# Kernel tuning notes

Hardware: AMD Instinct MI355X
Metric: run time of the kernel (lower is better)

The kernel has to match this reference:

```python
import jax, jax.numpy as jnp
import numpy as np

# ---- static config (matches init_kwargs) ----
OC, IC, K, S, PAD = 128, 64, 3, 1, 1
M, T, R = 5, 8, 2.5            # ALSH m, table_size, LSH bucket width r
SPAN = K * K * IC              # kernel_span = 576


def setup_inputs() -> dict:
    key = jax.random.key(0)
    k1, k2, k3, k4 = jax.random.split(key, 4)
    # xavier_uniform on the (OC, SPAN) kernel matrix
    bound = float(np.sqrt(6.0 / (OC + SPAN)))
    kernels = jax.random.uniform(k1, (OC, SPAN), minval=-bound, maxval=bound, dtype=jnp.float32)
    a = jax.random.normal(k2, (SPAN + M,), dtype=jnp.float32)          # LSH projection
    b = jax.random.uniform(k3, (), minval=0.0, maxval=R, dtype=jnp.float32)  # LSH offset
    x = jax.random.normal(k4, (16, IC, 56, 56), dtype=jnp.float32)
    return {"x": x, "kernels": kernels, "a": a, "b": b, "mode": 0}


def _im2col(x):
    # [B, SPAN, H2, W2] with feature order (C, kh, kw)
    p = jax.lax.conv_general_dilated_patches(x, (K, K), (S, S), [(PAD, PAD), (PAD, PAD)])
    B, _, H2, W2 = p.shape
    # patch matrix [SPAN, B*H2*W2]
    return p.transpose(1, 0, 2, 3).reshape(SPAN, -1), B, H2, W2


def _bucket(h):
    # floor((h+b)/r); fmod table_size; abs  (matches torch .fmod_ then .abs_)
    return jnp.abs(jnp.fmod(h.astype(jnp.int32), T))


def reference(x, kernels, a, b, mode):
    patch_matr, B, H2, W2 = _im2col(x)            # [SPAN, N], N = B*H2*W2

    # ---- vote: hash every patch column with Q-augmentation (append m halves) ----
    v = a[:SPAN] @ patch_matr + 0.5 * jnp.sum(a[SPAN:])      # [N]
    votes = _bucket(jnp.floor((v + b) / R))
    counts = jnp.zeros((T,), jnp.int32).at[votes].add(1)
    bucket = jnp.argmax(counts)                               # most common bucket

    # ---- hash table: hash each kernel row with P-augmentation (norm powers) ----
    norms2 = jnp.sum(kernels * kernels, axis=1)               # ||k||^2, [OC]
    powers = jnp.stack([norms2 ** (2 ** i) for i in range(M)], axis=1)  # ||k||^{2,4,...,2^M}
    hk = kernels @ a[:SPAN] + powers @ a[SPAN:]               # [OC]
    kidx = _bucket(jnp.floor((hk + b) / R))                   # bucket of each kernel

    # ---- select kernels in the winning bucket; scale by |rows|/OC ----
    mask = (kidx == bucket).astype(x.dtype)                   # [OC]
    cnt = jnp.sum(mask)
    # original gathers the selected rows (variable oc); we scatter back to the
    # full OC channels (zeros for inactive kernels) for static shapes.
    # empty bucket -> dense conv with all kernels, no rescale.
    factor = jnp.where(cnt > 0, mask * (OC / jnp.maximum(cnt, 1.0)), jnp.ones_like(mask))

    out = (kernels * factor[:, None]) @ patch_matr            # [OC, N]
    out = out.reshape(OC, B, H2 * W2).transpose(1, 0, 2)
    return out.reshape(B, OC, H2, W2)
```

## Files before the change

### kernel.cpp

```cpp
#include <hip/hip_runtime.h>
#include <math.h>

#define IC 64
#define OC 128
#define HH 56
#define WW 56
#define BATCH 16
#define HP 58
#define HW (HH*WW)
#define NPIX (BATCH*HW)
#define SPAN 576
#define TSIZE 8
#define VBANDS 28
#define VBLOCKS (BATCH*VBANDS)
#define W2BASE  VBLOCKS
#define BORDBASE (VBLOCKS + OC)
#define NBLK1 (BORDBASE + BATCH)

typedef unsigned short ushort_t;
typedef unsigned int uint_t;
typedef __attribute__((ext_vector_type(8))) __bf16 bf16x8;
typedef __attribute__((ext_vector_type(4))) float f32x4;

__device__ __forceinline__ ushort_t bf16_rne(float f) {
  uint_t u = __builtin_bit_cast(uint_t, f);
  u += 0x7FFFu + ((u >> 16) & 1u);
  return (ushort_t)(u >> 16);
}

__global__ __launch_bounds__(256)
void prep_kernel(const float* __restrict__ x, const float* __restrict__ kernels,
                 const float* __restrict__ a, const float* __restrict__ bptr,
                 ushort_t* __restrict__ xpad, ushort_t* __restrict__ w2m,
                 int* __restrict__ rbucket, int* __restrict__ hist_partial) {
  __shared__ float tl[224 * 9];
  __shared__ ushort_t lx[112 * 66];
  __shared__ int hist[TSIZE];
  __shared__ float red0[256], red1[256];
  const int bx = blockIdx.x, t = threadIdx.x;

  if (bx < VBLOCKS) {
    const int b = bx / VBANDS, band = bx % VBANDS;
    const int r0 = band * 2;
    if (t < TSIZE) hist[t] = 0;
    if (t < 224) {
      const int prow = r0 - 1 + t / 56;
      const int col = t % 56;
      const bool inr = ((unsigned)prow < (unsigned)HH);
      const bool mid = (t >= 56 && t < 168);
      const float* xb = x + (size_t)b * IC * HW + (inr ? prow * WW + col : 0);
      ushort_t* lxp = lx + (mid ? (t - 56) : 0) * 66;
      float t9[9] = {0, 0, 0, 0, 0, 0, 0, 0, 0};
      #pragma unroll 8
      for (int c = 0; c < IC; ++c) {
        float xv = inr ? xb[(size_t)c * HW] : 0.0f;
        #pragma unroll
        for (int tap = 0; tap < 9; ++tap) t9[tap] += a[c * 9 + tap] * xv;
        if (mid) lxp[c] = bf16_rne(xv);
      }
      #pragma unroll
      for (int tap = 0; tap < 9; ++tap) tl[t * 9 + tap] = t9[tap];
    }
    __syncthreads();
    if (t < 112) {
      int lr = t / 56, col = t % 56;
      float v = 0.0f;
      #pragma unroll
      for (int kh = 0; kh < 3; ++kh) {
        int gr = r0 + lr - 1 + kh;
        #pragma unroll
        for (int kw = 0; kw < 3; ++kw) {
          int cc = col - 1 + kw;
          if ((unsigned)gr < (unsigned)HH && (unsigned)cc < (unsigned)WW)
            v += tl[((lr + kh) * 56 + cc) * 9 + (kh * 3 + kw)];
        }
      }
      float tail = 0.5f * (a[576] + a[577] + a[578] + a[579] + a[580]);
      int hi = (int)floorf((v + tail + bptr[0]) / 2.5f);
      int r = hi % TSIZE;
      if (r < 0) r = -r;
      atomicAdd(&hist[r], 1);
    }
    {
      const uint_t* lxu = (const uint_t*)lx;
      uint_t* xp = (uint_t*)xpad;
      #pragma unroll
      for (int j = 0; j < 14; ++j) {
        int idx = j * 256 + t;
        int px = idx >> 5, cp = idx & 31;
        int lr = px / 56, c0 = px % 56;
        int y = r0 + 1 + lr, xw = c0 + 1;
        xp[(((size_t)(b * HP + y)) * HP + xw) * 32 + cp] = lxu[px * 33 + cp];
      }
    }
    __syncthreads();
    if (t < TSIZE) hist_partial[bx * TSIZE + t] = hist[t];
  } else if (bx < BORDBASE) {
    const int r = bx - W2BASE;
    const float* row = kernels + (size_t)r * SPAN;
    float d = 0.0f, n2 = 0.0f;
    #pragma unroll
    for (int k0 = 0; k0 < 3; ++k0) {
      int k = k0 * 256 + t;
      if (k < SPAN) { float kv = row[k]; d += kv * a[k]; n2 += kv * kv; }
    }
    red0[t] = d; red1[t] = n2;
    __syncthreads();
    for (int s = 128; s > 0; s >>= 1) {
      if (t < s) { red0[t] += red0[t + s]; red1[t] += red1[t + s]; }
      __syncthreads();
    }
    if (t == 0) {
      float hk = red0[0], p = red1[0];
      #pragma unroll
      for (int i = 0; i < 5; ++i) { hk += p * a[SPAN + i]; p = p * p; }
      int hi = (int)floorf((hk + bptr[0]) / 2.5f);
      int rr = hi % TSIZE;
      if (rr < 0) rr = -rr;
      rbucket[r] = rr;
    }
    #pragma unroll
    for (int j0 = 0; j0 < 3; ++j0) {
      int j = j0 * 256 + t;
      if (j < SPAN) {
        int tap = j / 64, rem = j % 64;
        int chunk = rem >> 3, c = rem & 7;
        w2m[(size_t)tap * 8192 + (r >> 4) * 1024 + chunk * 128 + (r & 15) * 8 + c] =
            bf16_rne(row[rem * 9 + tap]);
      }
    }
  } else {
    const int ib = bx - BORDBASE;
    uint_t* xp = (uint_t*)xpad + (size_t)ib * HP * HP * 32;
    for (int j = t; j < 7296; j += 256) {
      int px = j >> 5, cp = j & 31;
      int y, xw;
      if (px < 58) { y = 0; xw = px; }
      else if (px < 116) { y = 57; xw = px - 58; }
      else { int k = px - 116; y = 1 + (k >> 1); xw = (k & 1) * 57; }
      xp[((size_t)y * HP + xw) * 32 + cp] = 0;
    }
  }
}

__global__ __launch_bounds__(256, 4)
void gemm_kernel(const ushort_t* __restrict__ w2m, const ushort_t* __restrict__ xpad,
                 const int* __restrict__ hist_partial, const int* __restrict__ rbucket,
                 float* __restrict__ out) {
  __shared__ ushort_t As[8192];
  __shared__ ushort_t Bs[4096];
  __shared__ float factor_s[OC];
  __shared__ int counts_s[TSIZE];
  __shared__ int cnt_w[4];
  const int tid = threadIdx.x;
  const int wave = tid >> 6, lane = tid & 63;
  const int n0 = blockIdx.x * 64;

  int aseg[4];
  #pragma unroll
  for (int i = 0; i < 4; ++i) aseg[i] = (wave * 4 + i) * 512 + lane * 8;

  int bg;
  {
    int p = n0 + wave * 16 + (lane & 15);
    int b = p / HW, rem = p % HW;
    int h = rem / WW, w = rem % WW;
    bg = ((b * HP + h) * HP + w) * IC + (lane >> 4) * 8;
  }

  f32x4 acc[2][4] = {};

  for (int tap = 0; tap < 9; ++tap) {
    const int kh = tap / 3, kw = tap % 3;
    const int toffA = tap * 8192;
    const int toffB = (kh * HP + kw) * IC;
    __syncthreads();
    #pragma unroll
    for (int i = 0; i < 4; ++i)
      __builtin_amdgcn_global_load_lds(
          (const __attribute__((address_space(1))) void*)(w2m + toffA + aseg[i]),
          (__attribute__((address_space(3))) void*)(As + aseg[i]), 16, 0, 0);
    #pragma unroll
    for (int i = 0; i < 2; ++i)
      __builtin_amdgcn_global_load_lds(
          (const __attribute__((address_space(1))) void*)(xpad + bg + toffB + i * 32),
          (__attribute__((address_space(3))) void*)(Bs + wave * 1024 + i * 512 + lane * 8),
          16, 0, 0);
    __syncthreads();
    #pragma unroll
    for (int kk = 0; kk < 2; ++kk) {
      bf16x8 af[2], bfr[4];
      #pragma unroll
      for (int m = 0; m < 2; ++m)
        af[m] = *(const bf16x8*)(As + (wave * 2 + m) * 1024 + kk * 512 + lane * 8);
      #pragma unroll
      for (int n = 0; n < 4; ++n)
        bfr[n] = *(const bf16x8*)(Bs + n * 1024 + kk * 512 + lane * 8);
      #pragma unroll
      for (int m = 0; m < 2; ++m)
        #pragma unroll
        for (int n = 0; n < 4; ++n)
          acc[m][n] = __builtin_amdgcn_mfma_f32_16x16x32_bf16(af[m], bfr[n], acc[m][n], 0, 0, 0);
    }
  }

  if (tid < TSIZE) counts_s[tid] = 0;
  __syncthreads();
  {
    int bin = tid >> 5;
    int s = 0;
    for (int k = (tid & 31); k < VBLOCKS; k += 32) s += hist_partial[k * TSIZE + bin];
    atomicAdd(&counts_s[bin], s);
  }
  __syncthreads();
  int best = counts_s[0], bi = 0;
  #pragma unroll
  for (int i = 1; i < TSIZE; ++i) { int c = counts_s[i]; if (c > best) { best = c; bi = i; } }
  int isin = (tid < OC) ? ((rbucket[tid] == bi) ? 1 : 0) : 0;
  unsigned long long bal = __ballot(isin != 0);
  if (lane == 0) cnt_w[wave] = __popcll(bal);
  __syncthreads();
  int cnt = cnt_w[0] + cnt_w[1] + cnt_w[2] + cnt_w[3];
  if (tid < OC)
    factor_s[tid] = (cnt > 0) ? (isin ? 128.0f / (float)cnt : 0.0f) : 1.0f;
  __syncthreads();

  const int wm = wave * 32;
  #pragma unroll
  for (int n = 0; n < 4; ++n) {
    int np = n0 + n * 16 + (lane & 15);
    int b = np / HW;
    int rem = np % HW;
    float* obase = out + ((size_t)b * OC) * HW + rem;
    #pragma unroll
    for (int m = 0; m < 2; ++m) {
      int ocb = wm + m * 16 + (lane >> 4) * 4;
      #pragma unroll
      for (int r = 0; r < 4; ++r) {
        obase[(size_t)(ocb + r) * HW] = acc[m][n][r] * factor_s[ocb + r];
      }
    }
  }
}

extern "C" void kernel_launch(void* const* d_in, const int* in_sizes, int n_in,
                              void* d_out, int out_size, void* d_ws, size_t ws_size,
                              hipStream_t stream) {
  (void)in_sizes; (void)n_in; (void)out_size; (void)ws_size;
  const float* x = (const float*)d_in[0];
  const float* kernels = (const float*)d_in[1];
  const float* a = (const float*)d_in[2];
  const float* b = (const float*)d_in[3];
  float* out = (float*)d_out;

  char* ws = (char*)d_ws;
  int* rbucket = (int*)ws;
  int* hist_partial = (int*)(ws + 512);
  ushort_t* w2m = (ushort_t*)(ws + 16384);
  ushort_t* xpad = (ushort_t*)(ws + 16384 + 147456);

  prep_kernel<<<NBLK1, 256, 0, stream>>>(x, kernels, a, b, xpad, w2m, rbucket, hist_partial);
  gemm_kernel<<<NPIX / 64, 256, 0, stream>>>(w2m, xpad, hist_partial, rbucket, out);
}
```

Before: 116.0 us.

## Load GEMM fragments directly from global memory, dropping LDS staging

The GEMM kernel no longer stages weight and input tiles through shared memory with global_load_lds and two barriers per tap. Each wave now reads its bf16 A and B fragments straight from global memory (relying on L1/L2 caching), and the tap loop is unrolled by three. Launch bounds are relaxed to three blocks per SM to give the extra in-flight loads more registers. This removes the synchronisation and LDS round trip, but each B fragment is now fetched redundantly by all four waves and the loads become less coalesced.

```diff
diff --git a/kernel.cpp b/kernel.cpp
--- a/kernel.cpp
+++ b/kernel.cpp
@@ -143,12 +143,10 @@
   }
 }
 
-__global__ __launch_bounds__(256, 4)
+__global__ __launch_bounds__(256, 3)
 void gemm_kernel(const ushort_t* __restrict__ w2m, const ushort_t* __restrict__ xpad,
                  const int* __restrict__ hist_partial, const int* __restrict__ rbucket,
                  float* __restrict__ out) {
-  __shared__ ushort_t As[8192];
-  __shared__ ushort_t Bs[4096];
   __shared__ float factor_s[OC];
   __shared__ int counts_s[TSIZE];
   __shared__ int cnt_w[4];
@@ -156,46 +154,33 @@
   const int wave = tid >> 6, lane = tid & 63;
   const int n0 = blockIdx.x * 64;
 
-  int aseg[4];
+  const int abase = (wave * 2) * 1024 + lane * 8;
+
+  int pxb[4];
   #pragma unroll
-  for (int i = 0; i < 4; ++i) aseg[i] = (wave * 4 + i) * 512 + lane * 8;
-
-  int bg;
-  {
-    int p = n0 + wave * 16 + (lane & 15);
+  for (int n = 0; n < 4; ++n) {
+    int p = n0 + n * 16 + (lane & 15);
     int b = p / HW, rem = p % HW;
     int h = rem / WW, w = rem % WW;
-    bg = ((b * HP + h) * HP + w) * IC + (lane >> 4) * 8;
+    pxb[n] = ((b * HP + h) * HP + w) * IC + (lane >> 4) * 8;
   }
 
   f32x4 acc[2][4] = {};
 
+  #pragma unroll 3
   for (int tap = 0; tap < 9; ++tap) {
     const int kh = tap / 3, kw = tap % 3;
-    const int toffA = tap * 8192;
-    const int toffB = (kh * HP + kw) * IC;
-    __syncthreads();
-    #pragma unroll
-    for (int i = 0; i < 4; ++i)
-      __builtin_amdgcn_global_load_lds(
-          (const __attribute__((address_space(1))) void*)(w2m + toffA + aseg[i]),
-          (__attribute__((address_space(3))) void*)(As + aseg[i]), 16, 0, 0);
-    #pragma unroll
-    for (int i = 0; i < 2; ++i)
-      __builtin_amdgcn_global_load_lds(
-          (const __attribute__((address_space(1))) void*)(xpad + bg + toffB + i * 32),
-          (__attribute__((address_space(3))) void*)(Bs + wave * 1024 + i * 512 + lane * 8),
-          16, 0, 0);
-    __syncthreads();
+    const int aoff = tap * 8192 + abase;
+    const int boff = (kh * HP + kw) * IC;
     #pragma unroll
     for (int kk = 0; kk < 2; ++kk) {
       bf16x8 af[2], bfr[4];
       #pragma unroll
       for (int m = 0; m < 2; ++m)
-        af[m] = *(const bf16x8*)(As + (wave * 2 + m) * 1024 + kk * 512 + lane * 8);
+        af[m] = *(const bf16x8*)(w2m + aoff + m * 1024 + kk * 512);
       #pragma unroll
       for (int n = 0; n < 4; ++n)
-        bfr[n] = *(const bf16x8*)(Bs + n * 1024 + kk * 512 + lane * 8);
+        bfr[n] = *(const bf16x8*)(xpad + pxb[n] + boff + kk * 32);
       #pragma unroll
       for (int m = 0; m < 2; ++m)
         #pragma unroll
```

After: 141.0 us. 21.6% more time.
